# Kernel tuning notes

Measured on AMD Instinct MI355X. Metric: run time of the kernel, lower is better.

## Reference

```python
import jax, jax.numpy as jnp
import numpy as np

B, C3, Dz, H, W = 2, 128, 32, 24, 24
C2, K = 96, 8
E, NH = 256, 4
HD = E // NH
BETA_ADJ = 0.5
EPS = 1e-5
TOPO_HIDDEN = 64


def setup_inputs() -> dict:
    key = jax.random.key(0)
    ks = jax.random.split(key, 10)
    def n(k, shape, s=0.02):
        return jax.random.normal(k, shape, jnp.float32) * s
    return {
        "F3": jax.random.normal(ks[0], (B, C3, Dz, H, W), jnp.float32),
        "F2": jax.random.normal(ks[1], (B, C2, H, W, K), jnp.float32),
        "Wq": n(ks[2], (C3, E)),
        "Wk": n(ks[3], (C2, E)),
        "Wv": n(ks[4], (C2, E)),
        "Wp": n(ks[5], (E, C3)),
        "ln_q_g": jnp.ones((E,), jnp.float32),
        "ln_q_b": jnp.zeros((E,), jnp.float32),
        "ln_kv_g": jnp.ones((E,), jnp.float32),
        "ln_kv_b": jnp.zeros((E,), jnp.float32),
        "conv1_w": n(ks[6], (TOPO_HIDDEN, C2, 3, 3)),
        "bn_g": jnp.ones((TOPO_HIDDEN,), jnp.float32),
        "bn_b": jnp.zeros((TOPO_HIDDEN,), jnp.float32),
        "conv2_w": n(ks[7], (1, TOPO_HIDDEN, 1, 1)),
        "conv2_b": jnp.zeros((1,), jnp.float32),
        "lam": jnp.asarray(0.3, jnp.float32),
        "D0": 128,
        "slab": 16,
    }


def _layernorm(x, g, b):
    m = jnp.mean(x, -1, keepdims=True)
    v = jnp.mean(jnp.square(x - m), -1, keepdims=True)
    return (x - m) * jax.lax.rsqrt(v + EPS) * g + b


def _conv2d(x, w, pad):
    return jax.lax.conv_general_dilated(
        x, w, (1, 1), [(pad, pad), (pad, pad)],
        dimension_numbers=("NCHW", "OIHW", "NCHW"))


def _forward(F3, F2, Wq, Wk, Wv, Wp, ln_q_g, ln_q_b, ln_kv_g, ln_kv_b,
             conv1_w, bn_g, bn_b, conv2_w, conv2_b, lam, D0, slab):
    HW = H * W
    # static slab-index map (D0, slab are Python ints)
    z0 = np.round(np.linspace(0.0, D0 - 1, Dz)).astype(np.int64)
    k_index = np.clip(z0 // slab, 0, K - 1)

    # ---- TopoPriorHead2D (BatchNorm in eval mode, default running stats 0/1) ----
    f2_bkchw = jnp.transpose(F2, (0, 4, 1, 2, 3)).reshape(B * K, C2, H, W)
    h = _conv2d(f2_bkchw, conv1_w, 1)
    h = h * (bn_g / np.float32(np.sqrt(1.0 + EPS)))[None, :, None, None] + bn_b[None, :, None, None]
    h = jax.nn.relu(h)
    p_pred = _conv2d(h, conv2_w, 0) + conv2_b[None, :, None, None]  # [B*K,1,H,W]
    nei = jnp.ones((1, 1, 3, 3), jnp.float32).at[0, 0, 1, 1].set(0.0)
    ps_pred = _conv2d(p_pred, nei, 1)
    topo_map = (p_pred + 0.5 * ps_pred).reshape(B, K, HW)

    # ---- Q/K/V projections + LayerNorm ----
    x2 = jnp.transpose(F2, (0, 4, 2, 3, 1)).reshape(B, K, HW, C2)
    Kall = _layernorm(x2 @ Wk, ln_kv_g, ln_kv_b).reshape(B, K, HW, NH, HD)
    Vall = _layernorm(x2 @ Wv, ln_kv_g, ln_kv_b).reshape(B, K, HW, NH, HD)
    x3 = jnp.transpose(F3, (0, 2, 3, 4, 1)).reshape(B, Dz, HW, C3)
    Qall = _layernorm(x3 @ Wq, ln_q_g, ln_q_b).reshape(B, Dz, HW, NH, HD)

    Oh = jnp.zeros_like(Qall)
    scale = np.float32(1.0 / np.sqrt(HD))
    hw = np.arange(HW)
    for kk in range(K):
        z_ids = np.nonzero(k_index == kk)[0]
        if z_ids.size == 0:
            continue
        cand = [c for c in (kk - 1, kk, kk + 1) if 0 <= c < K]
        L = len(cand)
        slab_bias = jnp.asarray(np.concatenate(
            [np.full(HW, 0.0 if c == kk else -BETA_ADJ, np.float32) for c in cand]))
        Qg = Qall[:, z_ids]                                    # [B,Ds,HW,NH,HD]
        Kc = Kall[:, np.asarray(cand)].reshape(B, L * HW, NH, HD)
        Vc = Vall[:, np.asarray(cand)].reshape(B, L * HW, NH, HD)
        # [B,NH,Ds,HW,M]
        logits = jnp.einsum('bdphc,bmhc->bhdpm', Qg, Kc) * scale
        logits = logits + slab_bias
        # diagonal topo boost: query pixel p attends to same pixel p in slab cand[j]
        diag = jnp.zeros((B, HW, L * HW), logits.dtype)
        for j, c in enumerate(cand):
            diag = diag.at[:, hw, j * HW + hw].add(lam * topo_map[:, c])
        logits = logits + diag[:, None, None]
        attn = jax.nn.softmax(logits, axis=-1)
        Og = jnp.einsum('bhdpm,bmhc->bdphc', attn, Vc)         # [B,Ds,HW,NH,HD]
        Oh = Oh.at[:, z_ids].set(Og)

    Oall = Oh.reshape(B, Dz, HW, E) @ Wp                        # [B,D,HW,C3]
    Oall = jnp.transpose(Oall.reshape(B, Dz, H, W, C3), (0, 4, 1, 2, 3))
    return F3 + Oall


def reference(F3, F2, Wq, Wk, Wv, Wp, ln_q_g, ln_q_b, ln_kv_g, ln_kv_b,
              conv1_w, bn_g, bn_b, conv2_w, conv2_b, lam, D0, slab):
    return _forward(F3, F2, Wq, Wk, Wv, Wp, ln_q_g, ln_q_b, ln_kv_g, ln_kv_b,
                    conv1_w, bn_g, bn_b, conv2_w, conv2_b, lam, D0, slab)
```

## Files before the change

### kernel.cpp

```cpp
#include <hip/hip_runtime.h>

typedef float f32x4 __attribute__((ext_vector_type(4)));
typedef __bf16 bf16x8 __attribute__((ext_vector_type(8)));
typedef unsigned short ushort_t;

#define DEV_INLINE __device__ __forceinline__

constexpr int B_N  = 2;
constexpr int C3_N = 128;
constexpr int C2_N = 96;
constexpr int DZ_N = 32;
constexpr int H_N  = 24;
constexpr int W_N  = 24;
constexpr int K_N  = 8;
constexpr int E_N  = 256;
constexpr int HW_N = 576;

DEV_INLINE unsigned short f2bf(float x) {
  union { float f; unsigned u; } v; v.f = x;
  unsigned r = v.u + 0x7FFFu + ((v.u >> 16) & 1u);
  return (unsigned short)(r >> 16);
}

__global__ __launch_bounds__(384) void topo_conv1(
    const float* __restrict__ F2, const float* __restrict__ W1,
    float* __restrict__ Hp) {
  const int bid = blockIdx.x;
  const int cc = bid & 3;
  const int tg = (bid >> 2) & 3;
  const int bk = bid >> 4;
  const int b = bk >> 3, k = bk & 7;
  const int tid = threadIdx.x;
  const int y = tid >> 4;
  const int tq = tid & 15;

  __shared__ float simg[8][26][28];
  __shared__ float sw[16 * 97];

  float acc[24];
#pragma unroll
  for (int i = 0; i < 24; i++) acc[i] = 0.f;

  float* simgf = &simg[0][0][0];
  for (int i = tid; i < 8 * 26 * 28; i += 384) simgf[i] = 0.f;
  __syncthreads();

  for (int ch = 0; ch < 3; ch++) {
    if (ch) __syncthreads();
    const int c0 = cc * 24 + ch * 8;
    for (int i = tid; i < 8 * 24 * 24; i += 384) {
      int c = i / 576, p = i - c * 576;
      int yy = p / 24, xx = p - yy * 24;
      simg[c][yy + 1][xx + 1] =
          F2[(((b * C2_N + c0 + c) * H_N + yy) * W_N + xx) * K_N + k];
    }
    for (int i = tid; i < 16 * 72; i += 384) {
      int t2 = i / 72, rest = i - t2 * 72;
      int c = rest / 9, q = rest - c * 9;
      sw[t2 * 97 + c * 12 + q] =
          W1[(tg * 16 + t2) * (C2_N * 9) + (c0 + c) * 9 + q];
    }
    __syncthreads();
#pragma unroll 1
    for (int c = 0; c < 8; c++) {
      float w[9];
#pragma unroll
      for (int q = 0; q < 9; q++) w[q] = sw[tq * 97 + c * 12 + q];
#pragma unroll
      for (int dy = 0; dy < 3; dy++) {
        float r[26];
#pragma unroll
        for (int xx = 0; xx < 26; xx++) r[xx] = simg[c][y + dy][xx];
#pragma unroll
        for (int dx = 0; dx < 3; dx++) {
          float wv = w[dy * 3 + dx];
#pragma unroll
          for (int xx = 0; xx < 24; xx++)
            acc[xx] = fmaf(wv, r[xx + dx], acc[xx]);
        }
      }
    }
  }
  const int t = tg * 16 + tq;
  float* dst = &Hp[((cc * 16 + bk) * 64 + t) * HW_N + y * 24];
#pragma unroll
  for (int xx = 0; xx < 24; xx++) dst[xx] = acc[xx];
}

__global__ __launch_bounds__(576) void topo_mid(
    const float* __restrict__ Hp, const float* __restrict__ bn_g,
    const float* __restrict__ bn_b, const float* __restrict__ W2,
    float* __restrict__ part) {
  const int bid = blockIdx.x;
  const int tg = bid & 3, bk = bid >> 2;
  const int p = threadIdx.x;
  const float inv = rsqrtf(1.0f + 1e-5f);
  float acc = 0.f;
#pragma unroll 1
  for (int tt = 0; tt < 16; tt++) {
    const int t = tg * 16 + tt;
    float v = 0.f;
#pragma unroll
    for (int c4 = 0; c4 < 4; c4++)
      v += Hp[((c4 * 16 + bk) * 64 + t) * HW_N + p];
    acc = fmaf(W2[t], fmaxf(fmaf(bn_g[t] * inv, v, bn_b[t]), 0.f), acc);
  }
  part[(bk * 4 + tg) * HW_N + p] = acc;
}

__global__ __launch_bounds__(576) void topo_final2(
    const float* __restrict__ part, const float* __restrict__ b2,
    float* __restrict__ topo) {
  const int bk = blockIdx.x;
  const int p = threadIdx.x;
  __shared__ float pp[26][28];
  float* ppf = &pp[0][0];
  for (int i = p; i < 26 * 28; i += 576) ppf[i] = 0.f;
  float acc = b2[0];
#pragma unroll
  for (int tg = 0; tg < 4; tg++) acc += part[(bk * 4 + tg) * HW_N + p];
  __syncthreads();
  pp[p / 24 + 1][p % 24 + 1] = acc;
  __syncthreads();
  const int yy = p / 24 + 1, xx = p % 24 + 1;
  float s = pp[yy-1][xx-1] + pp[yy-1][xx] + pp[yy-1][xx+1]
          + pp[yy][xx-1]                  + pp[yy][xx+1]
          + pp[yy+1][xx-1] + pp[yy+1][xx] + pp[yy+1][xx+1];
  topo[bk * HW_N + p] = acc + 0.5f * s;
}

__global__ __launch_bounds__(256) void pack_all(
    const float* __restrict__ Wq, const float* __restrict__ Wk,
    const float* __restrict__ Wv, const float* __restrict__ Wp,
    ushort_t* __restrict__ Wqp, ushort_t* __restrict__ Wkp,
    ushort_t* __restrict__ Wvp, ushort_t* __restrict__ Wpp) {
  const int bblk = blockIdx.x, t = threadIdx.x;
  if (bblk < 256) {
    if (t < 128) Wqp[bblk * 128 + t] = f2bf(Wq[t * 256 + bblk]);
  } else if (bblk < 512) {
    const int n = bblk - 256;
    if (t < 96) Wkp[n * 96 + t] = f2bf(Wk[t * 256 + n]);
  } else if (bblk < 768) {
    const int n = bblk - 512;
    if (t < 96) Wvp[n * 96 + t] = f2bf(Wv[t * 256 + n]);
  } else {
    const int c = bblk - 768;
    Wpp[c * 256 + t] = f2bf(Wp[t * 128 + c]);
  }
}

template <int CIN, int MODE>
__global__ __launch_bounds__(256) void proj_mfma(
    const float* __restrict__ src, const ushort_t* __restrict__ Wpk,
    void* __restrict__ outp, const float* __restrict__ g,
    const float* __restrict__ bb,
    int outer, int bStride, int oStride, int pStride, int cStride) {
  __shared__ ushort_t sA[64 * 128];
  __shared__ int sRB[64];
  const int tid = threadIdx.x;
  const int rowG = blockIdx.x * 64;
  if (tid < 64) {
    int rr = rowG + tid;
    int b2 = rr / (outer * HW_N);
    int rem = rr - b2 * outer * HW_N;
    int o = rem / HW_N;
    int p = rem - o * HW_N;
    sRB[tid] = b2 * bStride + o * oStride + p * pStride;
  }
  __syncthreads();
  {
    const int r = tid & 63, kg = tid >> 6;
    constexpr int KC = CIN / 4;
    const float* s0 = src + sRB[r];
#pragma unroll
    for (int i = 0; i < KC; i += 2) {
      const int k = kg * KC + i;
      const float x0 = s0[k * cStride];
      const float x1 = s0[(k + 1) * cStride];
      const unsigned pr = (unsigned)f2bf(x0) | ((unsigned)f2bf(x1) << 16);
      ((unsigned*)sA)[r * 64 + (((k >> 3) + r) & 15) * 4 + ((k & 7) >> 1)] = pr;
    }
  }
  __syncthreads();
  const int wv = tid >> 6, lane = tid & 63;
  const int quad = lane >> 4, col = lane & 15;
  const int m = wv * 16 + col;
  constexpr int KS = CIN / 32;
  bf16x8 xb[KS];
#pragma unroll
  for (int ks = 0; ks < KS; ks++)
    xb[ks] = *(const bf16x8*)&sA[m * 128 + (((ks * 4 + quad) + m) & 15) * 8];
  f32x4 acc[16];
#pragma unroll
  for (int nt = 0; nt < 16; nt++) {
    const ushort_t* wrow = Wpk + (nt * 16 + col) * CIN + quad * 8;
    f32x4 a = (f32x4){0.f, 0.f, 0.f, 0.f};
#pragma unroll
    for (int ks = 0; ks < KS; ks++) {
      bf16x8 wf = *(const bf16x8*)&wrow[ks * 32];
      a = __builtin_amdgcn_mfma_f32_16x16x32_bf16(wf, xb[ks], a, 0, 0, 0);
    }
    acc[nt] = a;
  }
  const int mrow = rowG + m;
  if (MODE == 0) {
    float* dst = (float*)outp + (size_t)mrow * E_N;
#pragma unroll
    for (int nt = 0; nt < 16; nt++)
      *(f32x4*)&dst[nt * 16 + quad * 4] = acc[nt];
  } else {
    float s = 0.f;
#pragma unroll
    for (int nt = 0; nt < 16; nt++)
      s += acc[nt][0] + acc[nt][1] + acc[nt][2] + acc[nt][3];
    s += __shfl_xor(s, 16); s += __shfl_xor(s, 32);
    const float mean = s * (1.f / 256.f);
    float v = 0.f;
#pragma unroll
    for (int nt = 0; nt < 16; nt++)
#pragma unroll
      for (int r = 0; r < 4; r++) {
        const float d = acc[nt][r] - mean;
        v += d * d;
      }
    v += __shfl_xor(v, 16); v += __shfl_xor(v, 32);
    const float rstd = rsqrtf(v * (1.f / 256.f) + 1e-5f);
    if (MODE == 1) {
      const float QS = 0.18033688f;
      ushort_t* dst = (ushort_t*)outp + (size_t)mrow * E_N;
#pragma unroll
      for (int nt = 0; nt < 16; nt++) {
        const int n0 = nt * 16 + quad * 4;
        const float4 gv = *(const float4*)&g[n0];
        const float4 bv = *(const float4*)&bb[n0];
        ushort4 o;
        o.x = f2bf(QS * fmaf((acc[nt][0] - mean) * rstd, gv.x, bv.x));
        o.y = f2bf(QS * fmaf((acc[nt][1] - mean) * rstd, gv.y, bv.y));
        o.z = f2bf(QS * fmaf((acc[nt][2] - mean) * rstd, gv.z, bv.z));
        o.w = f2bf(QS * fmaf((acc[nt][3] - mean) * rstd, gv.w, bv.w));
        *(ushort4*)&dst[n0] = o;
      }
    } else {
      const int bk = mrow / HW_N;
      const int p = mrow - bk * HW_N;
      const int pc = p >> 6, mm = p & 63;
#pragma unroll
      for (int nt = 0; nt < 16; nt++) {
        const int n0 = nt * 16 + quad * 4;
        const float4 gv = *(const float4*)&g[n0];
        const float4 bv = *(const float4*)&bb[n0];
        ushort4 o;
        o.x = f2bf(fmaf((acc[nt][0] - mean) * rstd, gv.x, bv.x));
        o.y = f2bf(fmaf((acc[nt][1] - mean) * rstd, gv.y, bv.y));
        o.z = f2bf(fmaf((acc[nt][2] - mean) * rstd, gv.z, bv.z));
        o.w = f2bf(fmaf((acc[nt][3] - mean) * rstd, gv.w, bv.w));
        const int h = nt >> 2;
        const int grp = ((nt & 3) * 2 + (quad >> 1)) ^ (mm & 7);
        ushort_t* dst = (ushort_t*)outp +
            ((size_t)((bk * 4 + h) * 9 + pc)) * 4096 +
            mm * 64 + grp * 8 + (quad & 1) * 4;
        *(ushort4*)dst = o;
      }
    }
  }
}

__global__ __launch_bounds__(256) void pack_vt_ln(
    const float* __restrict__ Vraw, const float* __restrict__ g,
    const float* __restrict__ bb, ushort_t* __restrict__ Vtp) {
  const int bid = blockIdx.x;
  const int pc = bid % 9;
  const int bk = bid / 9;
  const int tid = threadIdx.x;
  __shared__ ushort_t sT[64][264];
  {
    const int m = tid >> 2, jj = tid & 3;
    const int row = bk * HW_N + pc * 64 + m;
    const float* src = &Vraw[(size_t)row * E_N + jj * 64];
    float4 xv[16];
    float s = 0.f;
#pragma unroll
    for (int i = 0; i < 16; i++) {
      xv[i] = *(const float4*)&src[i * 4];
      s += xv[i].x + xv[i].y + xv[i].z + xv[i].w;
    }
    s += __shfl_xor(s, 1); s += __shfl_xor(s, 2);
    const float mean = s * (1.f / 256.f);
    float v = 0.f;
#pragma unroll
    for (int i = 0; i < 16; i++) {
      xv[i].x -= mean; xv[i].y -= mean; xv[i].z -= mean; xv[i].w -= mean;
      v += xv[i].x * xv[i].x + xv[i].y * xv[i].y +
           xv[i].z * xv[i].z + xv[i].w * xv[i].w;
    }
    v += __shfl_xor(v, 1); v += __shfl_xor(v, 2);
    const float rstd = rsqrtf(v * (1.f / 256.f) + 1e-5f);
    ushort_t* drow = &sT[m][jj * 64];
#pragma unroll
    for (int i = 0; i < 16; i++) {
      const float4 gv = *(const float4*)&g[jj * 64 + i * 4];
      const float4 bv = *(const float4*)&bb[jj * 64 + i * 4];
      ushort4 o;
      o.x = f2bf(fmaf(xv[i].x * rstd, gv.x, bv.x));
      o.y = f2bf(fmaf(xv[i].y * rstd, gv.y, bv.y));
      o.z = f2bf(fmaf(xv[i].z * rstd, gv.z, bv.z));
      o.w = f2bf(fmaf(xv[i].w * rstd, gv.w, bv.w));
      *(ushort4*)&drow[i * 4] = o;
    }
  }
  __syncthreads();
  const int hh = tid >> 6, d = tid & 63;
  __attribute__((aligned(16))) ushort_t tmp[64];
#pragma unroll
  for (int k = 0; k < 64; k++) {
    const int pk = (k & 32) + ((k & 4) << 2) + ((k & 24) >> 1) + (k & 3);
    tmp[k] = sT[pk][hh * 64 + d];
  }
  const int chunk = (bk * 4 + hh) * 9 + pc;
  uint4* dst = (uint4*)&Vtp[chunk * 4096 + d * 64];
  const int sw = d & 7;
#pragma unroll
  for (int gg = 0; gg < 8; gg++) dst[gg ^ sw] = ((const uint4*)tmp)[gg];
}

__global__ __launch_bounds__(256) void attn_kernel(
    const ushort_t* __restrict__ Qbf, const ushort_t* __restrict__ Kpk,
    const ushort_t* __restrict__ Vtp, const float* __restrict__ topo,
    const float* __restrict__ lamp, const int* __restrict__ D0p,
    const int* __restrict__ slabp, ushort_t* __restrict__ Obf) {
  const int bid = blockIdx.x;
  const int hb = bid & 7;
  const int h = hb & 3, b = hb >> 2;
  const int zp = (bid >> 3) & 15;
  const int pb = bid >> 7;
  const int p0 = pb * 64;
  const int tid = threadIdx.x;
  const int w = tid >> 6, lane = tid & 63;
  const int quad = lane >> 4, col = lane & 15;
  const int z = zp * 2 + (w >> 1);
  const int th = w & 1;

  const float LOG2E = 1.44269504f;
  const float lam2 = lamp[0] * LOG2E;
  const int D0 = D0p[0], slab = slabp[0];
  const float step = (float)(D0 - 1) / (float)(DZ_N - 1);

  int kkw, kka, kkb;
  {
    int z0 = (int)floorf(fmaf((float)z, step, 0.5f));
    int kv = z0 / slab;
    kkw = kv < 0 ? 0 : (kv > K_N - 1 ? K_N - 1 : kv);
    int z0a = (int)floorf(fmaf((float)(zp * 2), step, 0.5f));
    int z0b = (int)floorf(fmaf((float)(zp * 2 + 1), step, 0.5f));
    int ka = z0a / slab; ka = ka < 0 ? 0 : (ka > K_N - 1 ? K_N - 1 : ka);
    int kb = z0b / slab; kb = kb < 0 ? 0 : (kb > K_N - 1 ? K_N - 1 : kb);
    kka = ka < kb ? ka : kb;
    kkb = ka < kb ? kb : ka;
  }
  const int c_lo = (kka - 1) < 0 ? 0 : (kka - 1);
  const int c_hi = (kkb + 1) > (K_N - 1) ? (K_N - 1) : (kkb + 1);

  __shared__ ushort_t sKV[2][8192];

  auto issue_fill = [&](int buf, int c, int pc) {
    const size_t cb = ((size_t)(((b * K_N + c) * 4 + h) * 9) + pc) * 4096;
#pragma unroll
    for (int j = 0; j < 4; j++) {
      const int seg = (w << 2) + j;
      const ushort_t* gsrc = (w < 2)
          ? (Kpk + cb + seg * 512 + lane * 8)
          : (Vtp + cb + (seg - 8) * 512 + lane * 8);
      ushort_t* ldst = &sKV[buf][seg * 512];
      __builtin_amdgcn_global_load_lds(
          (const __attribute__((address_space(1))) void*)gsrc,
          (__attribute__((address_space(3))) void*)ldst, 16, 0, 0);
    }
  };

  union { ushort_t u[8]; bf16x8 v; } uo;
#pragma unroll
  for (int i = 0; i < 8; i++) uo.u[i] = 0x3F80;
  const bf16x8 vone = uo.v;

  bf16x8 bq[2][2];
  const int qrow0 = (b * DZ_N + z) * HW_N + p0 + th * 32;
#pragma unroll
  for (int t = 0; t < 2; t++) {
    const ushort_t* qp = &Qbf[(qrow0 + t * 16 + col) * E_N + h * 64 + quad * 8];
    bq[t][0] = *(const bf16x8*)qp;
    bq[t][1] = *(const bf16x8*)(qp + 32);
  }

  f32x4 oacc[2][4];
#pragma unroll
  for (int t = 0; t < 2; t++)
#pragma unroll
    for (int dt = 0; dt < 4; dt++) oacc[t][dt] = (f32x4){0.f, 0.f, 0.f, 0.f};
  f32x4 lacc[2];
  lacc[0] = (f32x4){0.f, 0.f, 0.f, 0.f};
  lacc[1] = (f32x4){0.f, 0.f, 0.f, 0.f};

  const int s7 = col & 7;
  const int o1 = (quad ^ s7) * 8;
  const int o2 = ((quad + 4) ^ s7) * 8;

  int buf = 0;
  issue_fill(0, c_lo, 0);

  for (int c = c_lo; c <= c_hi; c++) {
    const bool act = (c >= kkw - 1) && (c <= kkw + 1);
    const float biasE2 = ((c == kkw) ? -20.0f : -20.5f) * LOG2E;
    const f32x4 bias4 = (f32x4){biasE2, biasE2, biasE2, biasE2};
    const float* topoc = &topo[(b * K_N + c) * HW_N + p0];
#pragma unroll 1
    for (int pc = 0; pc < 9; pc++) {
      __syncthreads();
      {
        int pc2 = pc + 1, c2 = c;
        if (pc2 == 9) { pc2 = 0; c2 = c + 1; }
        if (c2 <= c_hi) issue_fill(buf ^ 1, c2, pc2);
      }
      const ushort_t* sKb = &sKV[buf][0];
      const ushort_t* sVb = &sKV[buf][4096];
      buf ^= 1;
      if (!act) continue;

      bf16x8 ka[4][2];
#pragma unroll
      for (int kt = 0; kt < 4; kt++) {
        const ushort_t* kr = sKb + (kt * 16 + col) * 64;
        ka[kt][0] = *(const bf16x8*)(kr + o1);
        ka[kt][1] = *(const bf16x8*)(kr + o2);
      }

      bf16x8 pfrag[2][2];
#pragma unroll
      for (int t = 0; t < 2; t++) {
        f32x4 sv[4];
#pragma unroll
        for (int kt = 0; kt < 4; kt++) {
          f32x4 acc = __builtin_amdgcn_mfma_f32_16x16x32_bf16(
              ka[kt][0], bq[t][0], bias4, 0, 0, 0);
          acc = __builtin_amdgcn_mfma_f32_16x16x32_bf16(
              ka[kt][1], bq[t][1], acc, 0, 0, 0);
          sv[kt] = acc;
        }
        float xv[4][4];
#pragma unroll
        for (int kt = 0; kt < 4; kt++)
#pragma unroll
          for (int r = 0; r < 4; r++)
            xv[kt][r] = sv[kt][r];
        if (pc == pb) {
          const int ctt = th * 2 + t;
          const float tv2 = lam2 * topoc[th * 32 + t * 16 + col];
          const bool qok = ((col >> 2) == quad);
#pragma unroll
          for (int kt = 0; kt < 4; kt++)
#pragma unroll
            for (int r = 0; r < 4; r++)
              xv[kt][r] += (qok && kt == ctt && (col & 3) == r) ? tv2 : 0.f;
        }
        float ev[4][4];
#pragma unroll
        for (int kt = 0; kt < 4; kt++)
#pragma unroll
          for (int r = 0; r < 4; r++)
            ev[kt][r] = __builtin_amdgcn_exp2f(xv[kt][r]);
#pragma unroll
        for (int f = 0; f < 2; f++) {
          union { uint4 u; bf16x8 v; } pk;
          pk.u.x = __builtin_amdgcn_perm(__float_as_uint(ev[f*2][1]),
                                         __float_as_uint(ev[f*2][0]), 0x07060302u);
          pk.u.y = __builtin_amdgcn_perm(__float_as_uint(ev[f*2][3]),
                                         __float_as_uint(ev[f*2][2]), 0x07060302u);
          pk.u.z = __builtin_amdgcn_perm(__float_as_uint(ev[f*2+1][1]),
                                         __float_as_uint(ev[f*2+1][0]), 0x07060302u);
          pk.u.w = __builtin_amdgcn_perm(__float_as_uint(ev[f*2+1][3]),
                                         __float_as_uint(ev[f*2+1][2]), 0x07060302u);
          pfrag[t][f] = pk.v;
        }
        lacc[t] = __builtin_amdgcn_mfma_f32_16x16x32_bf16(
            vone, pfrag[t][0], lacc[t], 0, 0, 0);
        lacc[t] = __builtin_amdgcn_mfma_f32_16x16x32_bf16(
            vone, pfrag[t][1], lacc[t], 0, 0, 0);
      }

#pragma unroll
      for (int dt = 0; dt < 4; dt++) {
        const ushort_t* vr = sVb + (dt * 16 + col) * 64;
        bf16x8 va0 = *(const bf16x8*)(vr + o1);
        bf16x8 va1 = *(const bf16x8*)(vr + o2);
#pragma unroll
        for (int t = 0; t < 2; t++) {
          oacc[t][dt] = __builtin_amdgcn_mfma_f32_16x16x32_bf16(va0, pfrag[t][0], oacc[t][dt], 0, 0, 0);
          oacc[t][dt] = __builtin_amdgcn_mfma_f32_16x16x32_bf16(va1, pfrag[t][1], oacc[t][dt], 0, 0, 0);
        }
      }
    }
  }

#pragma unroll
  for (int t = 0; t < 2; t++) {
    const float invl = 1.f / lacc[t][0];
    const int row = qrow0 + t * 16 + col;
    ushort_t* orow = &Obf[(size_t)row * E_N + h * 64];
#pragma unroll
    for (int dt = 0; dt < 4; dt++) {
      ushort4 o;
      o.x = f2bf(oacc[t][dt][0] * invl);
      o.y = f2bf(oacc[t][dt][1] * invl);
      o.z = f2bf(oacc[t][dt][2] * invl);
      o.w = f2bf(oacc[t][dt][3] * invl);
      *(ushort4*)&orow[dt * 16 + quad * 4] = o;
    }
  }
}

__global__ __launch_bounds__(256) void out_proj_mfma(
    const ushort_t* __restrict__ Obf, const ushort_t* __restrict__ Wpp,
    const float* __restrict__ F3, float* __restrict__ outp) {
  __shared__ float sOut[64][129];
  const int tid = threadIdx.x;
  const int rowG = blockIdx.x * 64;
  const int wv = tid >> 6, lane = tid & 63;
  const int quad = lane >> 4, col = lane & 15;

  const ushort_t* xrow = &Obf[(size_t)(rowG + wv * 16 + col) * E_N + quad * 8];
  bf16x8 af[8];
#pragma unroll
  for (int ks = 0; ks < 8; ks++) af[ks] = *(const bf16x8*)&xrow[ks * 32];

#pragma unroll
  for (int nt = 0; nt < 8; nt++) {
    const ushort_t* wrow = &Wpp[(nt * 16 + col) * 256 + quad * 8];
    f32x4 a = (f32x4){0.f, 0.f, 0.f, 0.f};
#pragma unroll
    for (int ks = 0; ks < 8; ks++) {
      bf16x8 wf = *(const bf16x8*)&wrow[ks * 32];
      a = __builtin_amdgcn_mfma_f32_16x16x32_bf16(af[ks], wf, a, 0, 0, 0);
    }
#pragma unroll
    for (int r = 0; r < 4; r++)
      sOut[wv * 16 + quad * 4 + r][nt * 16 + col] = a[r];
  }
  __syncthreads();
  const int b = rowG / (DZ_N * HW_N);
  const int rem = rowG - b * DZ_N * HW_N;
  const int z = rem / HW_N;
  const int pp0 = rem - z * HW_N;
  const int pl = tid & 63, cg = tid >> 6;
  for (int c = cg * 32; c < cg * 32 + 32; c++) {
    const int gidx = ((b * C3_N + c) * DZ_N + z) * HW_N + pp0 + pl;
    outp[gidx] = F3[gidx] + sOut[pl][c];
  }
}

extern "C" void kernel_launch(void* const* d_in, const int* in_sizes, int n_in,
                              void* d_out, int out_size, void* d_ws, size_t ws_size,
                              hipStream_t stream) {
  (void)in_sizes; (void)n_in; (void)out_size; (void)ws_size;
  const float* F3      = (const float*)d_in[0];
  const float* F2      = (const float*)d_in[1];
  const float* Wq      = (const float*)d_in[2];
  const float* Wk      = (const float*)d_in[3];
  const float* Wv      = (const float*)d_in[4];
  const float* Wp      = (const float*)d_in[5];
  const float* ln_q_g  = (const float*)d_in[6];
  const float* ln_q_b  = (const float*)d_in[7];
  const float* ln_kv_g = (const float*)d_in[8];
  const float* ln_kv_b = (const float*)d_in[9];
  const float* conv1_w = (const float*)d_in[10];
  const float* bn_g    = (const float*)d_in[11];
  const float* bn_b    = (const float*)d_in[12];
  const float* conv2_w = (const float*)d_in[13];
  const float* conv2_b = (const float*)d_in[14];
  const float* lam     = (const float*)d_in[15];
  const int*   D0      = (const int*)d_in[16];
  const int*   slab    = (const int*)d_in[17];
  float* out = (float*)d_out;

  char* ws = (char*)d_ws;
  size_t off = 0;
  auto alloc = [&](size_t bytes) {
    void* p = ws + off;
    off += (bytes + 255) & ~(size_t)255;
    return p;
  };
  const int QROWS = B_N * DZ_N * HW_N;
  const int KVROWS = B_N * K_N * HW_N;
  ushort_t* Qbf = (ushort_t*)alloc((size_t)QROWS * E_N * 2);
  ushort_t* Kpk = (ushort_t*)alloc((size_t)KVROWS * E_N * 2);
  ushort_t* Vtp = (ushort_t*)alloc((size_t)KVROWS * E_N * 2);
  float* Vraw = (float*)alloc((size_t)KVROWS * E_N * 4);
  ushort_t* Obf = (ushort_t*)alloc((size_t)QROWS * E_N * 2);
  float* topo = (float*)alloc((size_t)B_N * K_N * HW_N * 4);
  float* part = (float*)alloc((size_t)64 * HW_N * 4);
  ushort_t* Wqp = (ushort_t*)alloc(256 * 128 * 2);
  ushort_t* Wkp = (ushort_t*)alloc(256 * 96 * 2);
  ushort_t* Wvp = (ushort_t*)alloc(256 * 96 * 2);
  ushort_t* Wpp = (ushort_t*)alloc(128 * 256 * 2);
  float* Hp = (float*)Obf;

  pack_all<<<896, 256, 0, stream>>>(Wq, Wk, Wv, Wp, Wqp, Wkp, Wvp, Wpp);
  topo_conv1<<<256, 384, 0, stream>>>(F2, conv1_w, Hp);
  topo_mid<<<64, 576, 0, stream>>>(Hp, bn_g, bn_b, conv2_w, part);
  topo_final2<<<16, 576, 0, stream>>>(part, conv2_b, topo);
  proj_mfma<128, 1><<<QROWS / 64, 256, 0, stream>>>(
      F3, Wqp, Qbf, ln_q_g, ln_q_b,
      DZ_N, C3_N * DZ_N * HW_N, HW_N, 1, DZ_N * HW_N);
  proj_mfma<96, 2><<<KVROWS / 64, 256, 0, stream>>>(
      F2, Wkp, Kpk, ln_kv_g, ln_kv_b,
      K_N, C2_N * HW_N * K_N, 1, K_N, HW_N * K_N);
  proj_mfma<96, 0><<<KVROWS / 64, 256, 0, stream>>>(
      F2, Wvp, Vraw, nullptr, nullptr,
      K_N, C2_N * HW_N * K_N, 1, K_N, HW_N * K_N);
  pack_vt_ln<<<B_N * K_N * 9, 256, 0, stream>>>(Vraw, ln_kv_g, ln_kv_b, Vtp);
  attn_kernel<<<1152, 256, 0, stream>>>(
      Qbf, Kpk, Vtp, topo, lam, D0, slab, Obf);
  out_proj_mfma<<<QROWS / 64, 256, 0, stream>>>(Obf, Wpp, F3, out);
}
```

Before: 326.8 us.

## Fuse K and V projections with LayerNorm and V transpose into one kernel

Replaces the separate K projection, V projection and V LayerNorm/transpose-pack kernels with a single proj_kv kernel. It loads each F2 tile once into shared memory, computes K and V with MFMA, applies LayerNorm in registers and writes the packed K and transposed V layouts directly. This drops two launches and the fp32 Vraw round trip through global memory. Separately, it adds s_setprio around the MFMA blocks in the attention kernel to favour matrix work while other waves do softmax.

After: 303.5 us. -7.1%, faster.

```diff
diff --git a/kernel.cpp b/kernel.cpp
--- a/kernel.cpp
+++ b/kernel.cpp
@@ -240,72 +240,138 @@
         o.w = f2bf(QS * fmaf((acc[nt][3] - mean) * rstd, gv.w, bv.w));
         *(ushort4*)&dst[n0] = o;
       }
-    } else {
-      const int bk = mrow / HW_N;
-      const int p = mrow - bk * HW_N;
-      const int pc = p >> 6, mm = p & 63;
-#pragma unroll
-      for (int nt = 0; nt < 16; nt++) {
-        const int n0 = nt * 16 + quad * 4;
-        const float4 gv = *(const float4*)&g[n0];
-        const float4 bv = *(const float4*)&bb[n0];
-        ushort4 o;
-        o.x = f2bf(fmaf((acc[nt][0] - mean) * rstd, gv.x, bv.x));
-        o.y = f2bf(fmaf((acc[nt][1] - mean) * rstd, gv.y, bv.y));
-        o.z = f2bf(fmaf((acc[nt][2] - mean) * rstd, gv.z, bv.z));
-        o.w = f2bf(fmaf((acc[nt][3] - mean) * rstd, gv.w, bv.w));
-        const int h = nt >> 2;
-        const int grp = ((nt & 3) * 2 + (quad >> 1)) ^ (mm & 7);
-        ushort_t* dst = (ushort_t*)outp +
-            ((size_t)((bk * 4 + h) * 9 + pc)) * 4096 +
-            mm * 64 + grp * 8 + (quad & 1) * 4;
-        *(ushort4*)dst = o;
-      }
-    }
-  }
-}
-
-__global__ __launch_bounds__(256) void pack_vt_ln(
-    const float* __restrict__ Vraw, const float* __restrict__ g,
-    const float* __restrict__ bb, ushort_t* __restrict__ Vtp) {
-  const int bid = blockIdx.x;
-  const int pc = bid % 9;
-  const int bk = bid / 9;
+    }
+  }
+}
+
+__global__ __launch_bounds__(256) void proj_kv(
+    const float* __restrict__ F2, const ushort_t* __restrict__ Wkp,
+    const ushort_t* __restrict__ Wvp, ushort_t* __restrict__ Kpk,
+    ushort_t* __restrict__ Vtp, const float* __restrict__ g,
+    const float* __restrict__ bb) {
+  __shared__ ushort_t sA[64 * 128];
+  __shared__ ushort_t sT[64][264];
   const int tid = threadIdx.x;
-  __shared__ ushort_t sT[64][264];
+  const int rowG = blockIdx.x * 64;
   {
-    const int m = tid >> 2, jj = tid & 3;
-    const int row = bk * HW_N + pc * 64 + m;
-    const float* src = &Vraw[(size_t)row * E_N + jj * 64];
-    float4 xv[16];
+    const int r = tid & 63, kg = tid >> 6;
+    const int rr = rowG + r;
+    const int b2 = rr / (K_N * HW_N);
+    const int rem = rr - b2 * (K_N * HW_N);
+    const int k = rem / HW_N;
+    const int p = rem - k * HW_N;
+    const float* s0 = F2 + (size_t)b2 * (C2_N * HW_N * K_N) + k + p * K_N;
+#pragma unroll
+    for (int i = 0; i < 24; i += 2) {
+      const int kk = kg * 24 + i;
+      const float x0 = s0[kk * (HW_N * K_N)];
+      const float x1 = s0[(kk + 1) * (HW_N * K_N)];
+      const unsigned pr = (unsigned)f2bf(x0) | ((unsigned)f2bf(x1) << 16);
+      ((unsigned*)sA)[r * 64 + (((kk >> 3) + r) & 15) * 4 + ((kk & 7) >> 1)] = pr;
+    }
+  }
+  __syncthreads();
+  const int wv = tid >> 6, lane = tid & 63;
+  const int quad = lane >> 4, col = lane & 15;
+  const int m = wv * 16 + col;
+  bf16x8 xb[3];
+#pragma unroll
+  for (int ks = 0; ks < 3; ks++)
+    xb[ks] = *(const bf16x8*)&sA[m * 128 + (((ks * 4 + quad) + m) & 15) * 8];
+
+  const int mrow = rowG + m;
+  const int bk = mrow / HW_N;
+  const int p = mrow - bk * HW_N;
+  const int pc = p >> 6, mm = p & 63;
+
+  {
+    f32x4 acc[16];
+#pragma unroll
+    for (int nt = 0; nt < 16; nt++) {
+      const ushort_t* wrow = Wkp + (nt * 16 + col) * 96 + quad * 8;
+      f32x4 a = (f32x4){0.f, 0.f, 0.f, 0.f};
+#pragma unroll
+      for (int ks = 0; ks < 3; ks++) {
+        bf16x8 wf = *(const bf16x8*)&wrow[ks * 32];
+        a = __builtin_amdgcn_mfma_f32_16x16x32_bf16(wf, xb[ks], a, 0, 0, 0);
+      }
+      acc[nt] = a;
+    }
     float s = 0.f;
 #pragma unroll
-    for (int i = 0; i < 16; i++) {
-      xv[i] = *(const float4*)&src[i * 4];
-      s += xv[i].x + xv[i].y + xv[i].z + xv[i].w;
-    }
-    s += __shfl_xor(s, 1); s += __shfl_xor(s, 2);
+    for (int nt = 0; nt < 16; nt++)
+      s += acc[nt][0] + acc[nt][1] + acc[nt][2] + acc[nt][3];
+    s += __shfl_xor(s, 16); s += __shfl_xor(s, 32);
     const float mean = s * (1.f / 256.f);
     float v = 0.f;
 #pragma unroll
-    for (int i = 0; i < 16; i++) {
-      xv[i].x -= mean; xv[i].y -= mean; xv[i].z -= mean; xv[i].w -= mean;
-      v += xv[i].x * xv[i].x + xv[i].y * xv[i].y +
-           xv[i].z * xv[i].z + xv[i].w * xv[i].w;
-    }
-    v += __shfl_xor(v, 1); v += __shfl_xor(v, 2);
+    for (int nt = 0; nt < 16; nt++)
+#pragma unroll
+      for (int r = 0; r < 4; r++) {
+        const float d = acc[nt][r] - mean;
+        v += d * d;
+      }
+    v += __shfl_xor(v, 16); v += __shfl_xor(v, 32);
     const float rstd = rsqrtf(v * (1.f / 256.f) + 1e-5f);
-    ushort_t* drow = &sT[m][jj * 64];
-#pragma unroll
-    for (int i = 0; i < 16; i++) {
-      const float4 gv = *(const float4*)&g[jj * 64 + i * 4];
-      const float4 bv = *(const float4*)&bb[jj * 64 + i * 4];
+#pragma unroll
+    for (int nt = 0; nt < 16; nt++) {
+      const int n0 = nt * 16 + quad * 4;
+      const float4 gv = *(const float4*)&g[n0];
+      const float4 bv = *(const float4*)&bb[n0];
       ushort4 o;
-      o.x = f2bf(fmaf(xv[i].x * rstd, gv.x, bv.x));
-      o.y = f2bf(fmaf(xv[i].y * rstd, gv.y, bv.y));
-      o.z = f2bf(fmaf(xv[i].z * rstd, gv.z, bv.z));
-      o.w = f2bf(fmaf(xv[i].w * rstd, gv.w, bv.w));
-      *(ushort4*)&drow[i * 4] = o;
+      o.x = f2bf(fmaf((acc[nt][0] - mean) * rstd, gv.x, bv.x));
+      o.y = f2bf(fmaf((acc[nt][1] - mean) * rstd, gv.y, bv.y));
+      o.z = f2bf(fmaf((acc[nt][2] - mean) * rstd, gv.z, bv.z));
+      o.w = f2bf(fmaf((acc[nt][3] - mean) * rstd, gv.w, bv.w));
+      const int h = nt >> 2;
+      const int grp = ((nt & 3) * 2 + (quad >> 1)) ^ (mm & 7);
+      ushort_t* dst = Kpk +
+          ((size_t)((bk * 4 + h) * 9 + pc)) * 4096 +
+          mm * 64 + grp * 8 + (quad & 1) * 4;
+      *(ushort4*)dst = o;
+    }
+  }
+
+  {
+    f32x4 acc[16];
+#pragma unroll
+    for (int nt = 0; nt < 16; nt++) {
+      const ushort_t* wrow = Wvp + (nt * 16 + col) * 96 + quad * 8;
+      f32x4 a = (f32x4){0.f, 0.f, 0.f, 0.f};
+#pragma unroll
+      for (int ks = 0; ks < 3; ks++) {
+        bf16x8 wf = *(const bf16x8*)&wrow[ks * 32];
+        a = __builtin_amdgcn_mfma_f32_16x16x32_bf16(wf, xb[ks], a, 0, 0, 0);
+      }
+      acc[nt] = a;
+    }
+    float s = 0.f;
+#pragma unroll
+    for (int nt = 0; nt < 16; nt++)
+      s += acc[nt][0] + acc[nt][1] + acc[nt][2] + acc[nt][3];
+    s += __shfl_xor(s, 16); s += __shfl_xor(s, 32);
+    const float mean = s * (1.f / 256.f);
+    float v = 0.f;
+#pragma unroll
+    for (int nt = 0; nt < 16; nt++)
+#pragma unroll
+      for (int r = 0; r < 4; r++) {
+        const float d = acc[nt][r] - mean;
+        v += d * d;
+      }
+    v += __shfl_xor(v, 16); v += __shfl_xor(v, 32);
+    const float rstd = rsqrtf(v * (1.f / 256.f) + 1e-5f);
+#pragma unroll
+    for (int nt = 0; nt < 16; nt++) {
+      const int n0 = nt * 16 + quad * 4;
+      const float4 gv = *(const float4*)&g[n0];
+      const float4 bv = *(const float4*)&bb[n0];
+      ushort4 o;
+      o.x = f2bf(fmaf((acc[nt][0] - mean) * rstd, gv.x, bv.x));
+      o.y = f2bf(fmaf((acc[nt][1] - mean) * rstd, gv.y, bv.y));
+      o.z = f2bf(fmaf((acc[nt][2] - mean) * rstd, gv.z, bv.z));
+      o.w = f2bf(fmaf((acc[nt][3] - mean) * rstd, gv.w, bv.w));
+      *(ushort4*)&sT[m][n0] = o;
     }
   }
   __syncthreads();
@@ -437,6 +503,7 @@
 #pragma unroll
       for (int t = 0; t < 2; t++) {
         f32x4 sv[4];
+        __builtin_amdgcn_s_setprio(1);
 #pragma unroll
         for (int kt = 0; kt < 4; kt++) {
           f32x4 acc = __builtin_amdgcn_mfma_f32_16x16x32_bf16(
@@ -445,6 +512,7 @@
               ka[kt][1], bq[t][1], acc, 0, 0, 0);
           sv[kt] = acc;
         }
+        __builtin_amdgcn_s_setprio(0);
         float xv[4][4];
 #pragma unroll
         for (int kt = 0; kt < 4; kt++)
@@ -486,6 +554,7 @@
             vone, pfrag[t][1], lacc[t], 0, 0, 0);
       }
 
+      __builtin_amdgcn_s_setprio(1);
 #pragma unroll
       for (int dt = 0; dt < 4; dt++) {
         const ushort_t* vr = sVb + (dt * 16 + col) * 64;
@@ -497,6 +566,7 @@
           oacc[t][dt] = __builtin_amdgcn_mfma_f32_16x16x32_bf16(va1, pfrag[t][1], oacc[t][dt], 0, 0, 0);
         }
       }
+      __builtin_amdgcn_s_setprio(0);
     }
   }
 
@@ -592,7 +662,6 @@
   ushort_t* Qbf = (ushort_t*)alloc((size_t)QROWS * E_N * 2);
   ushort_t* Kpk = (ushort_t*)alloc((size_t)KVROWS * E_N * 2);
   ushort_t* Vtp = (ushort_t*)alloc((size_t)KVROWS * E_N * 2);
-  float* Vraw = (float*)alloc((size_t)KVROWS * E_N * 4);
   ushort_t* Obf = (ushort_t*)alloc((size_t)QROWS * E_N * 2);
   float* topo = (float*)alloc((size_t)B_N * K_N * HW_N * 4);
   float* part = (float*)alloc((size_t)64 * HW_N * 4);
@@ -609,13 +678,8 @@
   proj_mfma<128, 1><<<QROWS / 64, 256, 0, stream>>>(
       F3, Wqp, Qbf, ln_q_g, ln_q_b,
       DZ_N, C3_N * DZ_N * HW_N, HW_N, 1, DZ_N * HW_N);
-  proj_mfma<96, 2><<<KVROWS / 64, 256, 0, stream>>>(
-      F2, Wkp, Kpk, ln_kv_g, ln_kv_b,
-      K_N, C2_N * HW_N * K_N, 1, K_N, HW_N * K_N);
-  proj_mfma<96, 0><<<KVROWS / 64, 256, 0, stream>>>(
-      F2, Wvp, Vraw, nullptr, nullptr,
-      K_N, C2_N * HW_N * K_N, 1, K_N, HW_N * K_N);
-  pack_vt_ln<<<B_N * K_N * 9, 256, 0, stream>>>(Vraw, ln_kv_g, ln_kv_b, Vtp);
+  proj_kv<<<KVROWS / 64, 256, 0, stream>>>(
+      F2, Wkp, Wvp, Kpk, Vtp, ln_kv_g, ln_kv_b);
   attn_kernel<<<1152, 256, 0, stream>>>(
       Qbf, Kpk, Vtp, topo, lam, D0, slab, Obf);
   out_proj_mfma<<<QROWS / 64, 256, 0, stream>>>(Obf, Wpp, F3, out);
```
